# Performance work log

Hardware: AMD Instinct MI355X
Metric: run time of the kernel (lower is better)

Reference implementation:

```python
import jax, jax.numpy as jnp
import numpy as np

POOL = 7
H, W, C = 200, 200, 512
NUM_ROIS = 128


def setup_inputs() -> dict:
    key = jax.random.key(0)
    k1, k2, k3 = jax.random.split(key, 3)
    img = jax.random.normal(k1, (1, H, W, C), dtype=jnp.float32)
    # (x, y, w, h) in feature-map pixels; w,h >= POOL+1 so every bin is >=1px,
    # and x+w <= W, y+h <= H so crops stay in bounds (as the original assumes).
    wh = jax.random.uniform(k2, (1, NUM_ROIS, 2), minval=float(POOL + 1), maxval=64.0)
    xy = jax.random.uniform(k3, (1, NUM_ROIS, 2)) * (jnp.array([W, H], jnp.float32) - wh)
    rois = jnp.concatenate([xy, wh], axis=-1).astype(jnp.float32)
    return {"img": img, "rois": rois, "pool_size": POOL}


def _roi_pool(x, rois, P):
    # x: (H, W, C) feature map; rois: (R, 4) as (x, y, w, h) floats.
    h_dim, w_dim, _ = x.shape
    ks = jnp.arange(P + 1, dtype=jnp.float32)
    rows = jnp.arange(h_dim)
    cols = jnp.arange(w_dim)

    def pool_one(roi):
        rx, ry, rw, rh = roi[0], roi[1], roi[2], roi[3]
        # Bin boundaries: original computes x1 = int(x + ix*w/P), x2 = int(x + (ix+1)*w/P),
        # i.e. contiguous non-overlapping segments [b[k], b[k+1]).
        bx = (rx + ks * (rw / P)).astype(jnp.int32)
        by = (ry + ks * (rh / P)).astype(jnp.int32)
        # Map each row/col to its bin id; out-of-roi pixels -> dummy segment P.
        rid = jnp.searchsorted(by, rows, side='right') - 1
        rid = jnp.where((rid < 0) | (rid >= P), P, rid)
        cid = jnp.searchsorted(bx, cols, side='right') - 1
        cid = jnp.where((cid < 0) | (cid >= P), P, cid)
        # Max-reduce rows into y-bins, then cols into x-bins (separable rect max).
        rm = jax.ops.segment_max(x, rid, num_segments=P + 1)                     # (P+1, W, C) [jy, w, c]
        cm = jax.ops.segment_max(rm.transpose(1, 0, 2), cid, num_segments=P + 1)  # (P+1, P+1, C) [ix, jy, c]
        return cm[:P, :P].transpose(1, 0, 2)  # (jy, ix, c)

    return jax.vmap(pool_one)(rois)  # (R, P, P, C)


def reference(img, rois, pool_size):
    # Output: (1, num_rois, pool_size, pool_size, channels), tf dim ordering.
    out = _roi_pool(img[0], rois[0], pool_size)
    return out[None]
```

## Files before the change

kernel.cpp:

```cpp
#include <hip/hip_runtime.h>


#define IMG_H 200
#define IMG_W 200
#define IMG_C 512
#define C4 (IMG_C / 4)
#define POOL 7
#define NROI 128

__device__ __forceinline__ float4 max4(float4 a, float4 b) {
    return make_float4(fmaxf(a.x, b.x), fmaxf(a.y, b.y),
                       fmaxf(a.z, b.z), fmaxf(a.w, b.w));
}

__global__ __launch_bounds__(128) void roi_pool_kernel(
    const float* __restrict__ img,
    const float* __restrict__ rois,
    float* __restrict__ out)
{
    const int bin = blockIdx.x % (POOL * POOL);
    const int roi = blockIdx.x / (POOL * POOL);
    const int jy = bin / POOL;
    const int ix = bin % POOL;

    const float rx = rois[roi * 4 + 0];
    const float ry = rois[roi * 4 + 1];
    const float rw = rois[roi * 4 + 2];
    const float rh = rois[roi * 4 + 3];

    const float sx = __fdiv_rn(rw, 7.0f);
    const float sy = __fdiv_rn(rh, 7.0f);
    const int x1 = (int)__fadd_rn(rx, __fmul_rn((float)ix,       sx));
    const int x2 = (int)__fadd_rn(rx, __fmul_rn((float)(ix + 1), sx));
    const int y1 = (int)__fadd_rn(ry, __fmul_rn((float)jy,       sy));
    const int y2 = (int)__fadd_rn(ry, __fmul_rn((float)(jy + 1), sy));

    const int c4 = threadIdx.x;
    const float4* __restrict__ img4 = (const float4*)img;

    float4 m0 = make_float4(-INFINITY, -INFINITY, -INFINITY, -INFINITY);
    float4 m1 = m0;

    int y = y1;
    for (; y + 2 <= y2; y += 2) {
        const float4* __restrict__ rowA = img4 + ((size_t)y       * IMG_W) * C4 + c4;
        const float4* __restrict__ rowB = img4 + ((size_t)(y + 1) * IMG_W) * C4 + c4;
        #pragma unroll 4
        for (int x = x1; x < x2; ++x) {
            float4 a = rowA[(size_t)x * C4];
            float4 b = rowB[(size_t)x * C4];
            m0 = max4(m0, a);
            m1 = max4(m1, b);
        }
    }
    if (y < y2) {
        const float4* __restrict__ rowA = img4 + ((size_t)y * IMG_W) * C4 + c4;
        #pragma unroll 4
        for (int x = x1; x < x2; ++x) {
            float4 a = rowA[(size_t)x * C4];
            m0 = max4(m0, a);
        }
    }
    float4 m = max4(m0, m1);

    float4* __restrict__ out4 = (float4*)out;
    out4[((size_t)(roi * POOL + jy) * POOL + ix) * C4 + c4] = m;
}

extern "C" void kernel_launch(void* const* d_in, const int* in_sizes, int n_in,
                              void* d_out, int out_size, void* d_ws, size_t ws_size,
                              hipStream_t stream) {
    (void)in_sizes; (void)n_in; (void)d_ws; (void)ws_size; (void)out_size;
    const float* img  = (const float*)d_in[0];
    const float* rois = (const float*)d_in[1];
    float* out = (float*)d_out;

    dim3 grid(NROI * POOL * POOL);
    dim3 block(128);
    roi_pool_kernel<<<grid, block, 0, stream>>>(img, rois, out);
}
```

Before: 142.8 us.

## Use persistent wavefronts with atomic work queue over quarter-channel bin tasks

Result: slower. 487.1 us (+241.0%).

```diff
diff --git a/kernel.cpp b/kernel.cpp
--- a/kernel.cpp
+++ b/kernel.cpp
@@ -7,75 +7,101 @@
 #define C4 (IMG_C / 4)
 #define POOL 7
 #define NROI 128
+#define NTASK (NROI * POOL * POOL * 4)
 
 __device__ __forceinline__ float4 max4(float4 a, float4 b) {
     return make_float4(fmaxf(a.x, b.x), fmaxf(a.y, b.y),
                        fmaxf(a.z, b.z), fmaxf(a.w, b.w));
 }
 
-__global__ __launch_bounds__(128) void roi_pool_kernel(
+__global__ __launch_bounds__(256) void roi_pool_persistent(
     const float* __restrict__ img,
     const float* __restrict__ rois,
-    float* __restrict__ out)
+    float* __restrict__ out,
+    unsigned int* __restrict__ queue)
 {
-    const int bin = blockIdx.x % (POOL * POOL);
-    const int roi = blockIdx.x / (POOL * POOL);
-    const int jy = bin / POOL;
-    const int ix = bin % POOL;
+    const int lane = threadIdx.x & 63;
+    const int p    = lane >> 5;
+    const int c    = lane & 31;
 
-    const float rx = rois[roi * 4 + 0];
-    const float ry = rois[roi * 4 + 1];
-    const float rw = rois[roi * 4 + 2];
-    const float rh = rois[roi * 4 + 3];
+    const float4* __restrict__ img4 = (const float4*)img;
+    float4* __restrict__ out4 = (float4*)out;
 
-    const float sx = __fdiv_rn(rw, 7.0f);
-    const float sy = __fdiv_rn(rh, 7.0f);
-    const int x1 = (int)__fadd_rn(rx, __fmul_rn((float)ix,       sx));
-    const int x2 = (int)__fadd_rn(rx, __fmul_rn((float)(ix + 1), sx));
-    const int y1 = (int)__fadd_rn(ry, __fmul_rn((float)jy,       sy));
-    const int y2 = (int)__fadd_rn(ry, __fmul_rn((float)(jy + 1), sy));
+    for (;;) {
+        unsigned int task;
+        if (lane == 0) task = atomicAdd(queue, 1u);
+        task = (unsigned int)__shfl((int)task, 0, 64);
+        if (task >= NTASK) break;
 
-    const int c4 = threadIdx.x;
-    const float4* __restrict__ img4 = (const float4*)img;
+        const int quarter = task & 3;
+        const int binroi  = task >> 2;
+        const int bin = binroi % (POOL * POOL);
+        const int roi = binroi / (POOL * POOL);
+        const int jy = bin / POOL;
+        const int ix = bin % POOL;
 
-    float4 m0 = make_float4(-INFINITY, -INFINITY, -INFINITY, -INFINITY);
-    float4 m1 = m0;
+        const float rx = rois[roi * 4 + 0];
+        const float ry = rois[roi * 4 + 1];
+        const float rw = rois[roi * 4 + 2];
+        const float rh = rois[roi * 4 + 3];
 
-    int y = y1;
-    for (; y + 2 <= y2; y += 2) {
-        const float4* __restrict__ rowA = img4 + ((size_t)y       * IMG_W) * C4 + c4;
-        const float4* __restrict__ rowB = img4 + ((size_t)(y + 1) * IMG_W) * C4 + c4;
-        #pragma unroll 4
-        for (int x = x1; x < x2; ++x) {
-            float4 a = rowA[(size_t)x * C4];
-            float4 b = rowB[(size_t)x * C4];
-            m0 = max4(m0, a);
-            m1 = max4(m1, b);
+        const float sx = __fdiv_rn(rw, 7.0f);
+        const float sy = __fdiv_rn(rh, 7.0f);
+        const int x1 = (int)__fadd_rn(rx, __fmul_rn((float)ix,       sx));
+        const int x2 = (int)__fadd_rn(rx, __fmul_rn((float)(ix + 1), sx));
+        const int y1 = (int)__fadd_rn(ry, __fmul_rn((float)jy,       sy));
+        const int y2 = (int)__fadd_rn(ry, __fmul_rn((float)(jy + 1), sy));
+
+        const int x2m1 = x2 - 1;
+        const int y2m1 = y2 - 1;
+        const int nx  = (x2 - x1 + 1) >> 1;
+        const int nyp = (y2 - y1 + 1) >> 1;
+
+        const float4* __restrict__ img4q = img4 + quarter * 32 + c;
+
+        float4 m0 = make_float4(-INFINITY, -INFINITY, -INFINITY, -INFINITY);
+        float4 m1 = m0;
+
+        for (int r = 0; r < nyp; ++r) {
+            const int yA = y1 + 2 * r;
+            const int yB = min(yA + 1, y2m1);
+            const float4* __restrict__ rowA = img4q + (size_t)yA * (IMG_W * C4);
+            const float4* __restrict__ rowB = img4q + (size_t)yB * (IMG_W * C4);
+            #pragma unroll 2
+            for (int k = 0; k < nx; ++k) {
+                int xx = x1 + 2 * k + p;
+                xx = min(xx, x2m1);
+                const size_t o = (size_t)xx * C4;
+                m0 = max4(m0, rowA[o]);
+                m1 = max4(m1, rowB[o]);
+            }
+        }
+        m0 = max4(m0, m1);
+
+        float4 res;
+        res.x = fmaxf(m0.x, __shfl_xor(m0.x, 32, 64));
+        res.y = fmaxf(m0.y, __shfl_xor(m0.y, 32, 64));
+        res.z = fmaxf(m0.z, __shfl_xor(m0.z, 32, 64));
+        res.w = fmaxf(m0.w, __shfl_xor(m0.w, 32, 64));
+
+        if (p == 0) {
+            out4[(size_t)((roi * (POOL * POOL) + bin) * C4) + quarter * 32 + c] = res;
         }
     }
-    if (y < y2) {
-        const float4* __restrict__ rowA = img4 + ((size_t)y * IMG_W) * C4 + c4;
-        #pragma unroll 4
-        for (int x = x1; x < x2; ++x) {
-            float4 a = rowA[(size_t)x * C4];
-            m0 = max4(m0, a);
-        }
-    }
-    float4 m = max4(m0, m1);
-
-    float4* __restrict__ out4 = (float4*)out;
-    out4[((size_t)(roi * POOL + jy) * POOL + ix) * C4 + c4] = m;
 }
 
 extern "C" void kernel_launch(void* const* d_in, const int* in_sizes, int n_in,
                               void* d_out, int out_size, void* d_ws, size_t ws_size,
                               hipStream_t stream) {
-    (void)in_sizes; (void)n_in; (void)d_ws; (void)ws_size; (void)out_size;
+    (void)in_sizes; (void)n_in; (void)ws_size; (void)out_size;
     const float* img  = (const float*)d_in[0];
     const float* rois = (const float*)d_in[1];
     float* out = (float*)d_out;
+    unsigned int* queue = (unsigned int*)d_ws;
 
-    dim3 grid(NROI * POOL * POOL);
-    dim3 block(128);
-    roi_pool_kernel<<<grid, block, 0, stream>>>(img, rois, out);
+    hipMemsetAsync(queue, 0, sizeof(unsigned int), stream);
+
+    dim3 grid(2048);
+    dim3 block(256);
+    roi_pool_persistent<<<grid, block, 0, stream>>>(img, rois, out, queue);
 }
```
